# Optimization experiments

Hardware: AMD Instinct MI355X
Metric: run time of the kernel (lower is better)

The kernel has to match this reference:

```python
import jax, jax.numpy as jnp
import numpy as np

T, H, E, K, I = 4096, 1024, 8, 2, 2048
EPS = 1e-5


def setup_inputs() -> dict:
    key = jax.random.key(0)
    ks = jax.random.split(key, 5)
    xavier = jax.nn.initializers.variance_scaling(1.0, 'fan_avg', 'uniform', dtype=jnp.float32)
    return {
        'x': jax.random.normal(ks[0], (T, H), dtype=jnp.float32),
        'scale': jnp.ones((H,), dtype=jnp.float32),
        'gate_kernel': xavier(ks[1], (H, E), jnp.float32),
        'gate_bias': jnp.zeros((E,), dtype=jnp.float32),
        'mlp1_weight': xavier(ks[2], (E, 2 * I, H), jnp.float32),
        'mlp1_bias': jnp.zeros((E, 2 * I), dtype=jnp.float32),
        'mlp2_weight': xavier(ks[3], (E, H, I), jnp.float32),
        'mlp2_bias': jnp.zeros((E, H), dtype=jnp.float32),
    }


def reference(x, scale, gate_kernel, gate_bias, mlp1_weight, mlp1_bias, mlp2_weight, mlp2_bias):
    # RMSNorm in fp32
    t = x.astype(jnp.float32)
    rms = jnp.sqrt(jnp.mean(t * t, axis=-1, keepdims=True) + EPS)
    normed = ((t / rms) * scale).astype(x.dtype)  # [T, H]

    # Gating: top-k experts + softmax over selected logits
    gate_logits = normed @ gate_kernel + gate_bias  # [T, E]
    expert_logits, expert_indices = jax.lax.top_k(gate_logits, K)  # [T, K]
    expert_weights = jax.nn.softmax(expert_logits, axis=-1)  # [T, K]

    # Dense all-expert SwiGLU MLP (faithful to vmap-over-experts original)
    # mlp1_weight: [E, 2I, H] -> mlp1: [E, T, 2I]
    mlp1 = jnp.einsum('td,efd->etf', normed, mlp1_weight) + mlp1_bias[:, None, :]
    gate_part = jnp.minimum(mlp1[..., :I], 7.0)
    linear_part = jnp.clip(mlp1[..., I:], -7.0, 7.0)
    swish_gate = gate_part * jax.nn.sigmoid(1.702 * gate_part)
    activated = swish_gate * (linear_part + 1.0)  # [E, T, I]
    # mlp2_weight: [E, H, I] -> expert_outputs: [T, E, H]
    expert_outputs = (jnp.einsum('eti,ehi->eth', activated, mlp2_weight)
                      + mlp2_bias[:, None, :]).transpose(1, 0, 2)

    # Scatter top-k weights to dense [T, E] and combine
    one_hot = jax.nn.one_hot(expert_indices, E, dtype=expert_outputs.dtype)  # [T, K, E]
    dense_gate_weights = jnp.sum(one_hot * expert_weights[..., None], axis=1)  # [T, E]
    fused = jnp.einsum('teh,te->th', expert_outputs, dense_gate_weights)
    return x + fused
```

## Files before the change

### kernel.cpp

```cpp
#include <hip/hip_runtime.h>
#include <hip/hip_bf16.h>
#include <math.h>

#define T_ 4096
#define H_ 1024
#define E_ 8
#define I_ 2048
#define EPS_ 1e-5f

using bf16x8 = __attribute__((ext_vector_type(8))) short;
using f32x4  = __attribute__((ext_vector_type(4))) float;

static __device__ __forceinline__ unsigned short f2bf(float f) {
    union { float f; unsigned int u; } v; v.f = f;
    unsigned int u = v.u;
    u += 0x7fffu + ((u >> 16) & 1u);
    return (unsigned short)(u >> 16);
}

static __device__ __forceinline__ void gld16(const unsigned short* g, unsigned short* l) {
    __builtin_amdgcn_global_load_lds(
        (const __attribute__((address_space(1))) unsigned int*)g,
        (__attribute__((address_space(3))) unsigned int*)l,
        16, 0, 0);
}

__global__ __launch_bounds__(256) void k_convert(
    const float* __restrict__ src, unsigned short* __restrict__ dst)
{
    size_t i = (size_t)blockIdx.x * 256 + threadIdx.x;
    const float4* s = (const float4*)src + i * 2;
    float4 a = s[0], b = s[1];
    ushort4 lo, hi;
    lo.x = f2bf(a.x); lo.y = f2bf(a.y); lo.z = f2bf(a.z); lo.w = f2bf(a.w);
    hi.x = f2bf(b.x); hi.y = f2bf(b.y); hi.z = f2bf(b.z); hi.w = f2bf(b.w);
    ((ushort4*)dst)[i * 2]     = lo;
    ((ushort4*)dst)[i * 2 + 1] = hi;
}

__global__ __launch_bounds__(256) void k_norm_gate(
    const float* __restrict__ x, const float* __restrict__ scale,
    const float* __restrict__ gk, const float* __restrict__ gb,
    unsigned short* __restrict__ normed_bf,
    int* __restrict__ counts, int* __restrict__ tok_list, float* __restrict__ wtok)
{
    int tid = threadIdx.x;
    int wave = tid >> 6, lane = tid & 63;
    int t = blockIdx.x * 4 + wave;
    const float* xr = x + (size_t)t * H_;
    int h0 = lane * 16;

    float4 xv[4], sv[4];
    #pragma unroll
    for (int c = 0; c < 4; c++) {
        xv[c] = *(const float4*)(xr + h0 + c * 4);
        sv[c] = *(const float4*)(scale + h0 + c * 4);
    }
    float ss = 0.f;
    #pragma unroll
    for (int c = 0; c < 4; c++)
        ss += xv[c].x*xv[c].x + xv[c].y*xv[c].y + xv[c].z*xv[c].z + xv[c].w*xv[c].w;
    #pragma unroll
    for (int off = 32; off; off >>= 1) ss += __shfl_xor(ss, off);
    float inv = 1.0f / sqrtf(ss / (float)H_ + EPS_);

    float nv[16];
    #pragma unroll
    for (int c = 0; c < 4; c++) {
        nv[c*4+0] = xv[c].x * inv * sv[c].x;
        nv[c*4+1] = xv[c].y * inv * sv[c].y;
        nv[c*4+2] = xv[c].z * inv * sv[c].z;
        nv[c*4+3] = xv[c].w * inv * sv[c].w;
    }
    #pragma unroll
    for (int c = 0; c < 4; c++) {
        ushort4 nb;
        nb.x = f2bf(nv[c*4+0]); nb.y = f2bf(nv[c*4+1]);
        nb.z = f2bf(nv[c*4+2]); nb.w = f2bf(nv[c*4+3]);
        *(ushort4*)(normed_bf + (size_t)t * H_ + h0 + c * 4) = nb;
    }

    float p[E_];
    #pragma unroll
    for (int e = 0; e < E_; e++) p[e] = 0.f;
    #pragma unroll
    for (int j = 0; j < 16; j++) {
        const float4* g4 = (const float4*)(gk + (size_t)(h0 + j) * E_);
        float4 a = g4[0], b = g4[1];
        float n = nv[j];
        p[0] += n*a.x; p[1] += n*a.y; p[2] += n*a.z; p[3] += n*a.w;
        p[4] += n*b.x; p[5] += n*b.y; p[6] += n*b.z; p[7] += n*b.w;
    }
    #pragma unroll
    for (int e = 0; e < E_; e++) {
        #pragma unroll
        for (int off = 32; off; off >>= 1) p[e] += __shfl_xor(p[e], off);
    }
    if (lane == 0) {
        int b0 = -1, b1 = -1; float l0 = -1e30f, l1 = -1e30f;
        #pragma unroll
        for (int e = 0; e < E_; e++) {
            float lg = p[e] + gb[e];
            if (lg > l0) { l1 = l0; b1 = b0; l0 = lg; b0 = e; }
            else if (lg > l1) { l1 = lg; b1 = e; }
        }
        float e1 = expf(l1 - l0);
        float w0 = 1.f / (1.f + e1);
        float w1 = e1 / (1.f + e1);
        wtok[t * 2 + 0] = w0;
        wtok[t * 2 + 1] = w1;
        int p0 = atomicAdd(&counts[b0], 1);
        tok_list[b0 * T_ + p0] = t * 2 + 0;
        int p1 = atomicAdd(&counts[b1], 1);
        tok_list[b1 * T_ + p1] = t * 2 + 1;
    }
}

__global__ __launch_bounds__(256) void k_mlp1(
    const unsigned short* __restrict__ w1b,
    const float* __restrict__ b1,
    const unsigned short* __restrict__ normed_bf,
    const int* __restrict__ counts, const int* __restrict__ tok_list,
    unsigned short* __restrict__ act)
{
    int e = blockIdx.z;
    int Ne = counts[e];
    int mt0 = blockIdx.y * 128;
    if (mt0 >= Ne) return;
    int it0 = blockIdx.x * 64;
    int tid = threadIdx.x;
    int lane = tid & 63, w = tid >> 6;
    int quad = lane >> 4, m16 = lane & 15;
    int wr = w >> 1, wc = w & 1;

    __shared__ unsigned short lA[2][128 * 64];
    __shared__ unsigned short lBg[2][64 * 64];
    __shared__ unsigned short lBl[2][64 * 64];
    __shared__ int ls_tk[128];

    if (tid < 128) {
        int slot = mt0 + tid;
        ls_tk[tid] = (slot < Ne) ? tok_list[e * T_ + slot] : -1;
    }

    int lr = lane >> 3;
    int pc = lane & 7;

    const unsigned short* srcA[4];
    #pragma unroll
    for (int it = 0; it < 4; it++) {
        int r = w * 32 + it * 8 + lr;
        int slot = mt0 + r;
        int tk = (slot < Ne) ? tok_list[e * T_ + slot] : 0;
        srcA[it] = normed_bf + (size_t)(tk >> 1) * H_ + ((pc ^ (r & 7)) << 3);
    }
    const size_t w1base = (size_t)e * 2 * I_ * H_;
    const unsigned short* srcG[2];
    const unsigned short* srcL[2];
    #pragma unroll
    for (int it = 0; it < 2; it++) {
        int r = w * 16 + it * 8 + lr;
        srcG[it] = w1b + w1base + (size_t)(it0 + r) * H_ + ((pc ^ (r & 7)) << 3);
        srcL[it] = srcG[it] + (size_t)I_ * H_;
    }

    f32x4 accg[4][2], accl[4][2];
    #pragma unroll
    for (int mi = 0; mi < 4; mi++)
        #pragma unroll
        for (int ni = 0; ni < 2; ni++) {
            accg[mi][ni] = (f32x4){0.f, 0.f, 0.f, 0.f};
            accl[mi][ni] = (f32x4){0.f, 0.f, 0.f, 0.f};
        }

    int m7 = m16 & 7;

#define STAGE1(buf, kk)                                                       \
    {                                                                          \
        _Pragma("unroll")                                                      \
        for (int it = 0; it < 4; it++)                                         \
            gld16(srcA[it] + (kk), &lA[buf][(w * 32 + it * 8) * 64]);          \
        _Pragma("unroll")                                                      \
        for (int it = 0; it < 2; it++) {                                       \
            gld16(srcG[it] + (kk), &lBg[buf][(w * 16 + it * 8) * 64]);         \
            gld16(srcL[it] + (kk), &lBl[buf][(w * 16 + it * 8) * 64]);         \
        }                                                                      \
    }

#define COMP1(buf)                                                             \
    {                                                                          \
        _Pragma("unroll")                                                      \
        for (int ks = 0; ks < 2; ks++) {                                       \
            int jj = ks * 4 + quad;                                            \
            bf16x8 af[4], bg[2], bl[2];                                        \
            _Pragma("unroll")                                                  \
            for (int mi = 0; mi < 4; mi++)                                     \
                af[mi] = *(const bf16x8*)(&lA[buf][(wr * 64 + mi * 16 + m16) * 64 + ((jj ^ m7) << 3)]); \
            _Pragma("unroll")                                                  \
            for (int ni = 0; ni < 2; ni++) {                                   \
                bg[ni] = *(const bf16x8*)(&lBg[buf][(wc * 32 + ni * 16 + m16) * 64 + ((jj ^ m7) << 3)]); \
                bl[ni] = *(const bf16x8*)(&lBl[buf][(wc * 32 + ni * 16 + m16) * 64 + ((jj ^ m7) << 3)]); \
            }                                                                  \
            _Pragma("unroll")                                                  \
            for (int mi = 0; mi < 4; mi++)                                     \
                _Pragma("unroll")                                              \
                for (int ni = 0; ni < 2; ni++) {                               \
                    accg[mi][ni] = __builtin_amdgcn_mfma_f32_16x16x32_bf16(    \
                        af[mi], bg[ni], accg[mi][ni], 0, 0, 0);                \
                    accl[mi][ni] = __builtin_amdgcn_mfma_f32_16x16x32_bf16(    \
                        af[mi], bl[ni], accl[mi][ni], 0, 0, 0);                \
                }                                                              \
        }                                                                      \
    }

    STAGE1(0, 0);
    __syncthreads();
    for (int kk = 0; kk < H_; kk += 128) {
        STAGE1(1, kk + 64);
        COMP1(0);
        __syncthreads();
        if (kk + 128 < H_) STAGE1(0, kk + 128);
        COMP1(1);
        __syncthreads();
    }
#undef STAGE1
#undef COMP1

    const float* b1g = b1 + (size_t)e * 2 * I_;
    const float* b1l = b1g + I_;
    #pragma unroll
    for (int mi = 0; mi < 4; mi++) {
        #pragma unroll
        for (int reg = 0; reg < 4; reg++) {
            int row = wr * 64 + mi * 16 + quad * 4 + reg;
            int tk = ls_tk[row];
            if (tk < 0) continue;
            #pragma unroll
            for (int ni = 0; ni < 2; ni++) {
                int i = it0 + wc * 32 + ni * 16 + m16;
                float g = accg[mi][ni][reg] + b1g[i];
                float l = accl[mi][ni][reg] + b1l[i];
                g = fminf(g, 7.f);
                l = fminf(fmaxf(l, -7.f), 7.f);
                float sw = g / (1.f + expf(-1.702f * g));
                act[(size_t)tk * I_ + i] = f2bf(sw * (l + 1.f));
            }
        }
    }
}

__global__ __launch_bounds__(256) void k_mlp2(
    const unsigned short* __restrict__ w2b,
    const float* __restrict__ b2,
    const unsigned short* __restrict__ act,
    const int* __restrict__ counts, const int* __restrict__ tok_list,
    float* __restrict__ ybuf)
{
    int e = blockIdx.z;
    int Ne = counts[e];
    int mt0 = blockIdx.y * 128;
    if (mt0 >= Ne) return;
    int ht0 = blockIdx.x * 128;
    int tid = threadIdx.x;
    int lane = tid & 63, w = tid >> 6;
    int quad = lane >> 4, m16 = lane & 15;
    int wr = w >> 1, wc = w & 1;

    __shared__ unsigned short lA[2][128 * 64];
    __shared__ unsigned short lB[2][128 * 64];
    __shared__ int ls_tk[128];

    if (tid < 128) {
        int slot = mt0 + tid;
        ls_tk[tid] = (slot < Ne) ? tok_list[e * T_ + slot] : -1;
    }

    int lr = lane >> 3;
    int pc = lane & 7;

    const unsigned short* srcA[4];
    #pragma unroll
    for (int it = 0; it < 4; it++) {
        int r = w * 32 + it * 8 + lr;
        int slot = mt0 + r;
        int tk = (slot < Ne) ? tok_list[e * T_ + slot] : 0;
        srcA[it] = act + (size_t)tk * I_ + ((pc ^ (r & 7)) << 3);
    }
    const size_t w2base = (size_t)e * H_ * I_;
    const unsigned short* srcB[4];
    #pragma unroll
    for (int it = 0; it < 4; it++) {
        int r = w * 32 + it * 8 + lr;
        srcB[it] = w2b + w2base + (size_t)(ht0 + r) * I_ + ((pc ^ (r & 7)) << 3);
    }

    f32x4 acc[4][4];
    #pragma unroll
    for (int mi = 0; mi < 4; mi++)
        #pragma unroll
        for (int ni = 0; ni < 4; ni++)
            acc[mi][ni] = (f32x4){0.f, 0.f, 0.f, 0.f};

    int m7 = m16 & 7;

#define STAGE2(buf, kk)                                                       \
    {                                                                          \
        _Pragma("unroll")                                                      \
        for (int it = 0; it < 4; it++)                                         \
            gld16(srcA[it] + (kk), &lA[buf][(w * 32 + it * 8) * 64]);          \
        _Pragma("unroll")                                                      \
        for (int it = 0; it < 4; it++)                                         \
            gld16(srcB[it] + (kk), &lB[buf][(w * 32 + it * 8) * 64]);          \
    }

#define COMP2(buf)                                                             \
    {                                                                          \
        _Pragma("unroll")                                                      \
        for (int ks = 0; ks < 2; ks++) {                                       \
            int jj = ks * 4 + quad;                                            \
            bf16x8 af[4], bv[4];                                               \
            _Pragma("unroll")                                                  \
            for (int mi = 0; mi < 4; mi++)                                     \
                af[mi] = *(const bf16x8*)(&lA[buf][(wr * 64 + mi * 16 + m16) * 64 + ((jj ^ m7) << 3)]); \
            _Pragma("unroll")                                                  \
            for (int ni = 0; ni < 4; ni++)                                     \
                bv[ni] = *(const bf16x8*)(&lB[buf][(wc * 64 + ni * 16 + m16) * 64 + ((jj ^ m7) << 3)]); \
            _Pragma("unroll")                                                  \
            for (int mi = 0; mi < 4; mi++)                                     \
                _Pragma("unroll")                                              \
                for (int ni = 0; ni < 4; ni++)                                 \
                    acc[mi][ni] = __builtin_amdgcn_mfma_f32_16x16x32_bf16(     \
                        af[mi], bv[ni], acc[mi][ni], 0, 0, 0);                 \
        }                                                                      \
    }

    STAGE2(0, 0);
    __syncthreads();
    for (int kk = 0; kk < I_; kk += 128) {
        STAGE2(1, kk + 64);
        COMP2(0);
        __syncthreads();
        if (kk + 128 < I_) STAGE2(0, kk + 128);
        COMP2(1);
        __syncthreads();
    }
#undef STAGE2
#undef COMP2

    const float* b2e = b2 + (size_t)e * H_;
    #pragma unroll
    for (int mi = 0; mi < 4; mi++) {
        #pragma unroll
        for (int reg = 0; reg < 4; reg++) {
            int row = wr * 64 + mi * 16 + quad * 4 + reg;
            int tk = ls_tk[row];
            if (tk < 0) continue;
            #pragma unroll
            for (int ni = 0; ni < 4; ni++) {
                int h = ht0 + wc * 64 + ni * 16 + m16;
                ybuf[(size_t)tk * H_ + h] = acc[mi][ni][reg] + b2e[h];
            }
        }
    }
}

__global__ __launch_bounds__(256) void k_combine(
    const float* __restrict__ x, const float* __restrict__ ybuf,
    const float* __restrict__ wtok, float* __restrict__ out)
{
    int t = blockIdx.x;
    int tid = threadIdx.x;
    float w0 = wtok[t * 2 + 0];
    float w1 = wtok[t * 2 + 1];
    float4 xv = ((const float4*)(x + (size_t)t * H_))[tid];
    float4 y0 = ((const float4*)(ybuf + (size_t)(t * 2) * H_))[tid];
    float4 y1 = ((const float4*)(ybuf + (size_t)(t * 2 + 1) * H_))[tid];
    float4 o;
    o.x = xv.x + w0 * y0.x + w1 * y1.x;
    o.y = xv.y + w0 * y0.y + w1 * y1.y;
    o.z = xv.z + w0 * y0.z + w1 * y1.z;
    o.w = xv.w + w0 * y0.w + w1 * y1.w;
    ((float4*)(out + (size_t)t * H_))[tid] = o;
}

extern "C" void kernel_launch(void* const* d_in, const int* in_sizes, int n_in,
                              void* d_out, int out_size, void* d_ws, size_t ws_size,
                              hipStream_t stream) {
    const float* x     = (const float*)d_in[0];
    const float* scale = (const float*)d_in[1];
    const float* gk    = (const float*)d_in[2];
    const float* gb    = (const float*)d_in[3];
    const float* w1    = (const float*)d_in[4];
    const float* b1    = (const float*)d_in[5];
    const float* w2    = (const float*)d_in[6];
    const float* b2    = (const float*)d_in[7];
    float* out = (float*)d_out;

    char* ws = (char*)d_ws;
    const size_t MB = 1024 * 1024;
    unsigned short* normed_bf = (unsigned short*)ws;
    unsigned short* act       = (unsigned short*)(ws + 8 * MB);
    unsigned short* w1b       = (unsigned short*)(ws + 40 * MB);
    float*          ybuf      = (float*)(ws + 40 * MB);
    unsigned short* w2b       = (unsigned short*)(ws + 104 * MB);
    char* ctl                 = ws + 136 * MB;
    int*   counts   = (int*)ctl;
    int*   tok_list = (int*)(ctl + 256);
    float* wtok     = (float*)(ctl + 256 + (size_t)E_ * T_ * 4);

    hipMemsetAsync(counts, 0, E_ * sizeof(int), stream);

    k_norm_gate<<<dim3(T_ / 4), dim3(256), 0, stream>>>(
        x, scale, gk, gb, normed_bf, counts, tok_list, wtok);
    k_convert<<<dim3((E_ * 2 * I_ * H_) / (256 * 8)), dim3(256), 0, stream>>>(w1, w1b);
    k_convert<<<dim3((E_ * H_ * I_) / (256 * 8)), dim3(256), 0, stream>>>(w2, w2b);

    k_mlp1<<<dim3(I_ / 64, T_ / 128, E_), dim3(256), 0, stream>>>(
        w1b, b1, normed_bf, counts, tok_list, act);
    k_mlp2<<<dim3(H_ / 128, T_ / 128, E_), dim3(256), 0, stream>>>(
        w2b, b2, act, counts, tok_list, ybuf);
    k_combine<<<dim3(T_), dim3(256), 0, stream>>>(x, ybuf, wtok, out);
}
```

Measured before the change: 609.1 us.

## Enlarge MoE GEMM tiles to 512 threads with ping-pong MFMA scheduling

Both expert GEMM kernels move to 512-thread blocks with 256-row token tiles. mlp1 now computes 128 gate plus 128 linear columns per block in one merged B buffer. The K loop is restructured so each wave splits its MFMA work into sub-blocks separated by raw s_barrier calls, with setprio raised around MFMAs and explicit vmcnt waits, to interleave LDS reads, global prefetch and matrix math across waves. The larger tiles are meant to raise operand reuse and hide latency, at the cost of more LDS per block, more registers, lower occupancy and more wasted rows for experts whose token counts do not fill a tile.

```diff
diff --git a/kernel.cpp b/kernel.cpp
--- a/kernel.cpp
+++ b/kernel.cpp
@@ -24,6 +24,8 @@
         (__attribute__((address_space(3))) unsigned int*)l,
         16, 0, 0);
 }
+
+#define BAR() __builtin_amdgcn_s_barrier()
 
 __global__ __launch_bounds__(256) void k_convert(
     const float* __restrict__ src, unsigned short* __restrict__ dst)
@@ -116,7 +118,7 @@
     }
 }
 
-__global__ __launch_bounds__(256) void k_mlp1(
+__global__ __launch_bounds__(512) void k_mlp1(
     const unsigned short* __restrict__ w1b,
     const float* __restrict__ b1,
     const unsigned short* __restrict__ normed_bf,
@@ -125,20 +127,20 @@
 {
     int e = blockIdx.z;
     int Ne = counts[e];
-    int mt0 = blockIdx.y * 128;
+    int mt0 = blockIdx.y * 256;
     if (mt0 >= Ne) return;
-    int it0 = blockIdx.x * 64;
+    int it0 = blockIdx.x * 128;
     int tid = threadIdx.x;
     int lane = tid & 63, w = tid >> 6;
     int quad = lane >> 4, m16 = lane & 15;
-    int wr = w >> 1, wc = w & 1;
-
-    __shared__ unsigned short lA[2][128 * 64];
-    __shared__ unsigned short lBg[2][64 * 64];
-    __shared__ unsigned short lBl[2][64 * 64];
-    __shared__ int ls_tk[128];
-
-    if (tid < 128) {
+    int wr = w >> 2, wc = w & 3;
+    int m7 = m16 & 7;
+
+    __shared__ unsigned short lA[2][256 * 64];
+    __shared__ unsigned short lB[2][256 * 64];
+    __shared__ int ls_tk[256];
+
+    if (tid < 256) {
         int slot = mt0 + tid;
         ls_tk[tid] = (slot < Ne) ? tok_list[e * T_ + slot] : -1;
     }
@@ -155,101 +157,115 @@
         srcA[it] = normed_bf + (size_t)(tk >> 1) * H_ + ((pc ^ (r & 7)) << 3);
     }
     const size_t w1base = (size_t)e * 2 * I_ * H_;
-    const unsigned short* srcG[2];
-    const unsigned short* srcL[2];
-    #pragma unroll
-    for (int it = 0; it < 2; it++) {
-        int r = w * 16 + it * 8 + lr;
-        srcG[it] = w1b + w1base + (size_t)(it0 + r) * H_ + ((pc ^ (r & 7)) << 3);
-        srcL[it] = srcG[it] + (size_t)I_ * H_;
-    }
-
-    f32x4 accg[4][2], accl[4][2];
-    #pragma unroll
-    for (int mi = 0; mi < 4; mi++)
-        #pragma unroll
-        for (int ni = 0; ni < 2; ni++) {
-            accg[mi][ni] = (f32x4){0.f, 0.f, 0.f, 0.f};
-            accl[mi][ni] = (f32x4){0.f, 0.f, 0.f, 0.f};
-        }
-
-    int m7 = m16 & 7;
-
-#define STAGE1(buf, kk)                                                       \
+    const unsigned short* srcB[4];
+    #pragma unroll
+    for (int it = 0; it < 4; it++) {
+        int r = w * 32 + it * 8 + lr;
+        int col = it0 + ((r >> 6) << 5) + (r & 31);
+        const unsigned short* base = w1b + w1base + ((r & 32) ? (size_t)I_ * H_ : (size_t)0);
+        srcB[it] = base + (size_t)col * H_ + ((pc ^ (r & 7)) << 3);
+    }
+
+    f32x4 acc[8][4];
+    #pragma unroll
+    for (int mi = 0; mi < 8; mi++)
+        #pragma unroll
+        for (int ni = 0; ni < 4; ni++)
+            acc[mi][ni] = (f32x4){0.f, 0.f, 0.f, 0.f};
+
+#define STAGE1(b, koff)                                                        \
     {                                                                          \
         _Pragma("unroll")                                                      \
         for (int it = 0; it < 4; it++)                                         \
-            gld16(srcA[it] + (kk), &lA[buf][(w * 32 + it * 8) * 64]);          \
-        _Pragma("unroll")                                                      \
-        for (int it = 0; it < 2; it++) {                                       \
-            gld16(srcG[it] + (kk), &lBg[buf][(w * 16 + it * 8) * 64]);         \
-            gld16(srcL[it] + (kk), &lBl[buf][(w * 16 + it * 8) * 64]);         \
-        }                                                                      \
-    }
-
-#define COMP1(buf)                                                             \
-    {                                                                          \
-        _Pragma("unroll")                                                      \
-        for (int ks = 0; ks < 2; ks++) {                                       \
-            int jj = ks * 4 + quad;                                            \
-            bf16x8 af[4], bg[2], bl[2];                                        \
+            gld16(srcA[it] + (koff), &lA[b][(w * 32 + it * 8) * 64]);          \
+        _Pragma("unroll")                                                      \
+        for (int it = 0; it < 4; it++)                                         \
+            gld16(srcB[it] + (koff), &lB[b][(w * 32 + it * 8) * 64]);          \
+        __builtin_amdgcn_sched_barrier(0);                                     \
+    }
+
+#define RD_A1(dst, b, pm)                                                      \
+    _Pragma("unroll")                                                          \
+    for (int i = 0; i < 4; i++)                                                \
+        _Pragma("unroll")                                                      \
+        for (int ks = 0; ks < 2; ks++)                                         \
+            dst[i][ks] = *(const bf16x8*)(&lA[b][(wr * 128 + ((pm) * 4 + i) * 16 + m16) * 64 + (((ks * 4 + quad) ^ m7) << 3)]);
+
+#define RD_B1(dst, b, pn)                                                      \
+    _Pragma("unroll")                                                          \
+    for (int i = 0; i < 2; i++)                                                \
+        _Pragma("unroll")                                                      \
+        for (int ks = 0; ks < 2; ks++)                                         \
+            dst[i][ks] = *(const bf16x8*)(&lB[b][(wc * 64 + ((pn) * 2 + i) * 16 + m16) * 64 + (((ks * 4 + quad) ^ m7) << 3)]);
+
+#define MM1(pm, pn, bsrc)                                                      \
+    {                                                                          \
+        __builtin_amdgcn_s_setprio(1);                                         \
+        _Pragma("unroll")                                                      \
+        for (int i = 0; i < 4; i++)                                            \
             _Pragma("unroll")                                                  \
-            for (int mi = 0; mi < 4; mi++)                                     \
-                af[mi] = *(const bf16x8*)(&lA[buf][(wr * 64 + mi * 16 + m16) * 64 + ((jj ^ m7) << 3)]); \
-            _Pragma("unroll")                                                  \
-            for (int ni = 0; ni < 2; ni++) {                                   \
-                bg[ni] = *(const bf16x8*)(&lBg[buf][(wc * 32 + ni * 16 + m16) * 64 + ((jj ^ m7) << 3)]); \
-                bl[ni] = *(const bf16x8*)(&lBl[buf][(wc * 32 + ni * 16 + m16) * 64 + ((jj ^ m7) << 3)]); \
-            }                                                                  \
-            _Pragma("unroll")                                                  \
-            for (int mi = 0; mi < 4; mi++)                                     \
+            for (int j = 0; j < 2; j++)                                        \
                 _Pragma("unroll")                                              \
-                for (int ni = 0; ni < 2; ni++) {                               \
-                    accg[mi][ni] = __builtin_amdgcn_mfma_f32_16x16x32_bf16(    \
-                        af[mi], bg[ni], accg[mi][ni], 0, 0, 0);                \
-                    accl[mi][ni] = __builtin_amdgcn_mfma_f32_16x16x32_bf16(    \
-                        af[mi], bl[ni], accl[mi][ni], 0, 0, 0);                \
-                }                                                              \
-        }                                                                      \
+                for (int ks = 0; ks < 2; ks++)                                 \
+                    acc[(pm) * 4 + i][(pn) * 2 + j] =                          \
+                        __builtin_amdgcn_mfma_f32_16x16x32_bf16(               \
+                            am[i][ks], bsrc[j][ks],                            \
+                            acc[(pm) * 4 + i][(pn) * 2 + j], 0, 0, 0);         \
+        __builtin_amdgcn_s_setprio(0);                                         \
+    }
+
+#define KTILE1(b, do_stage, koff)                                              \
+    {                                                                          \
+        bf16x8 am[4][2], bn0[2][2], bn1[2][2];                                 \
+        RD_A1(am, b, 0); RD_B1(bn0, b, 0);                                     \
+        if (do_stage) STAGE1(1 - (b), koff);                                   \
+        BAR(); MM1(0, 0, bn0); BAR();                                          \
+        RD_B1(bn1, b, 1);                                                      \
+        BAR(); MM1(0, 1, bn1); BAR();                                          \
+        RD_A1(am, b, 1);                                                       \
+        BAR(); MM1(1, 1, bn1); BAR();                                          \
+        MM1(1, 0, bn0);                                                        \
+        asm volatile("s_waitcnt vmcnt(0)" ::: "memory");                       \
+        __builtin_amdgcn_sched_barrier(0);                                     \
+        BAR();                                                                 \
     }
 
     STAGE1(0, 0);
     __syncthreads();
-    for (int kk = 0; kk < H_; kk += 128) {
-        STAGE1(1, kk + 64);
-        COMP1(0);
-        __syncthreads();
-        if (kk + 128 < H_) STAGE1(0, kk + 128);
-        COMP1(1);
-        __syncthreads();
+    for (int t2 = 0; t2 < 16; t2 += 2) {
+        KTILE1(0, true, (t2 + 1) * 64);
+        KTILE1(1, (t2 + 2) < 16, (t2 + 2) * 64);
     }
 #undef STAGE1
-#undef COMP1
+#undef RD_A1
+#undef RD_B1
+#undef MM1
+#undef KTILE1
 
     const float* b1g = b1 + (size_t)e * 2 * I_;
     const float* b1l = b1g + I_;
     #pragma unroll
-    for (int mi = 0; mi < 4; mi++) {
+    for (int mi = 0; mi < 8; mi++) {
         #pragma unroll
         for (int reg = 0; reg < 4; reg++) {
-            int row = wr * 64 + mi * 16 + quad * 4 + reg;
+            int row = wr * 128 + mi * 16 + quad * 4 + reg;
             int tk = ls_tk[row];
             if (tk < 0) continue;
             #pragma unroll
-            for (int ni = 0; ni < 2; ni++) {
-                int i = it0 + wc * 32 + ni * 16 + m16;
-                float g = accg[mi][ni][reg] + b1g[i];
-                float l = accl[mi][ni][reg] + b1l[i];
+            for (int j = 0; j < 2; j++) {
+                int c = it0 + wc * 32 + j * 16 + m16;
+                float g = acc[mi][j][reg]     + b1g[c];
+                float l = acc[mi][2 + j][reg] + b1l[c];
                 g = fminf(g, 7.f);
                 l = fminf(fmaxf(l, -7.f), 7.f);
                 float sw = g / (1.f + expf(-1.702f * g));
-                act[(size_t)tk * I_ + i] = f2bf(sw * (l + 1.f));
+                act[(size_t)tk * I_ + c] = f2bf(sw * (l + 1.f));
             }
         }
     }
 }
 
-__global__ __launch_bounds__(256) void k_mlp2(
+__global__ __launch_bounds__(512) void k_mlp2(
     const unsigned short* __restrict__ w2b,
     const float* __restrict__ b2,
     const unsigned short* __restrict__ act,
@@ -258,19 +274,20 @@
 {
     int e = blockIdx.z;
     int Ne = counts[e];
-    int mt0 = blockIdx.y * 128;
+    int mt0 = blockIdx.y * 256;
     if (mt0 >= Ne) return;
     int ht0 = blockIdx.x * 128;
     int tid = threadIdx.x;
     int lane = tid & 63, w = tid >> 6;
     int quad = lane >> 4, m16 = lane & 15;
     int wr = w >> 1, wc = w & 1;
-
-    __shared__ unsigned short lA[2][128 * 64];
+    int m7 = m16 & 7;
+
+    __shared__ unsigned short lA[2][256 * 64];
     __shared__ unsigned short lB[2][128 * 64];
-    __shared__ int ls_tk[128];
-
-    if (tid < 128) {
+    __shared__ int ls_tk[256];
+
+    if (tid < 256) {
         int slot = mt0 + tid;
         ls_tk[tid] = (slot < Ne) ? tok_list[e * T_ + slot] : -1;
     }
@@ -287,10 +304,10 @@
         srcA[it] = act + (size_t)tk * I_ + ((pc ^ (r & 7)) << 3);
     }
     const size_t w2base = (size_t)e * H_ * I_;
-    const unsigned short* srcB[4];
-    #pragma unroll
-    for (int it = 0; it < 4; it++) {
-        int r = w * 32 + it * 8 + lr;
+    const unsigned short* srcB[2];
+    #pragma unroll
+    for (int it = 0; it < 2; it++) {
+        int r = w * 16 + it * 8 + lr;
         srcB[it] = w2b + w2base + (size_t)(ht0 + r) * I_ + ((pc ^ (r & 7)) << 3);
     }
 
@@ -301,51 +318,70 @@
         for (int ni = 0; ni < 4; ni++)
             acc[mi][ni] = (f32x4){0.f, 0.f, 0.f, 0.f};
 
-    int m7 = m16 & 7;
-
-#define STAGE2(buf, kk)                                                       \
+#define STAGE2(b, koff)                                                        \
     {                                                                          \
         _Pragma("unroll")                                                      \
         for (int it = 0; it < 4; it++)                                         \
-            gld16(srcA[it] + (kk), &lA[buf][(w * 32 + it * 8) * 64]);          \
-        _Pragma("unroll")                                                      \
-        for (int it = 0; it < 4; it++)                                         \
-            gld16(srcB[it] + (kk), &lB[buf][(w * 32 + it * 8) * 64]);          \
-    }
-
-#define COMP2(buf)                                                             \
-    {                                                                          \
-        _Pragma("unroll")                                                      \
-        for (int ks = 0; ks < 2; ks++) {                                       \
-            int jj = ks * 4 + quad;                                            \
-            bf16x8 af[4], bv[4];                                               \
+            gld16(srcA[it] + (koff), &lA[b][(w * 32 + it * 8) * 64]);          \
+        _Pragma("unroll")                                                      \
+        for (int it = 0; it < 2; it++)                                         \
+            gld16(srcB[it] + (koff), &lB[b][(w * 16 + it * 8) * 64]);          \
+        __builtin_amdgcn_sched_barrier(0);                                     \
+    }
+
+#define RD_A2(dst, b)                                                          \
+    _Pragma("unroll")                                                          \
+    for (int i = 0; i < 4; i++)                                                \
+        _Pragma("unroll")                                                      \
+        for (int ks = 0; ks < 2; ks++)                                         \
+            dst[i][ks] = *(const bf16x8*)(&lA[b][(wr * 64 + i * 16 + m16) * 64 + (((ks * 4 + quad) ^ m7) << 3)]);
+
+#define RD_B2(dst, b, pn)                                                      \
+    _Pragma("unroll")                                                          \
+    for (int i = 0; i < 2; i++)                                                \
+        _Pragma("unroll")                                                      \
+        for (int ks = 0; ks < 2; ks++)                                         \
+            dst[i][ks] = *(const bf16x8*)(&lB[b][(wc * 64 + ((pn) * 2 + i) * 16 + m16) * 64 + (((ks * 4 + quad) ^ m7) << 3)]);
+
+#define MM2(pn, bsrc)                                                          \
+    {                                                                          \
+        __builtin_amdgcn_s_setprio(1);                                         \
+        _Pragma("unroll")                                                      \
+        for (int i = 0; i < 4; i++)                                            \
             _Pragma("unroll")                                                  \
-            for (int mi = 0; mi < 4; mi++)                                     \
-                af[mi] = *(const bf16x8*)(&lA[buf][(wr * 64 + mi * 16 + m16) * 64 + ((jj ^ m7) << 3)]); \
-            _Pragma("unroll")                                                  \
-            for (int ni = 0; ni < 4; ni++)                                     \
-                bv[ni] = *(const bf16x8*)(&lB[buf][(wc * 64 + ni * 16 + m16) * 64 + ((jj ^ m7) << 3)]); \
-            _Pragma("unroll")                                                  \
-            for (int mi = 0; mi < 4; mi++)                                     \
+            for (int j = 0; j < 2; j++)                                        \
                 _Pragma("unroll")                                              \
-                for (int ni = 0; ni < 4; ni++)                                 \
-                    acc[mi][ni] = __builtin_amdgcn_mfma_f32_16x16x32_bf16(     \
-                        af[mi], bv[ni], acc[mi][ni], 0, 0, 0);                 \
-        }                                                                      \
+                for (int ks = 0; ks < 2; ks++)                                 \
+                    acc[i][(pn) * 2 + j] =                                     \
+                        __builtin_amdgcn_mfma_f32_16x16x32_bf16(               \
+                            am[i][ks], bsrc[j][ks], acc[i][(pn) * 2 + j], 0, 0, 0); \
+        __builtin_amdgcn_s_setprio(0);                                         \
+    }
+
+#define KTILE2(b, do_stage, koff)                                              \
+    {                                                                          \
+        bf16x8 am[4][2], bn0[2][2], bn1[2][2];                                 \
+        RD_A2(am, b); RD_B2(bn0, b, 0);                                        \
+        if (do_stage) STAGE2(1 - (b), koff);                                   \
+        BAR(); MM2(0, bn0); BAR();                                             \
+        RD_B2(bn1, b, 1);                                                      \
+        BAR(); MM2(1, bn1);                                                    \
+        asm volatile("s_waitcnt vmcnt(0)" ::: "memory");                       \
+        __builtin_amdgcn_sched_barrier(0);                                     \
+        BAR();                                                                 \
     }
 
     STAGE2(0, 0);
     __syncthreads();
-    for (int kk = 0; kk < I_; kk += 128) {
-        STAGE2(1, kk + 64);
-        COMP2(0);
-        __syncthreads();
-        if (kk + 128 < I_) STAGE2(0, kk + 128);
-        COMP2(1);
-        __syncthreads();
+    for (int t2 = 0; t2 < 32; t2 += 2) {
+        KTILE2(0, true, (t2 + 1) * 64);
+        KTILE2(1, (t2 + 2) < 32, (t2 + 2) * 64);
     }
 #undef STAGE2
-#undef COMP2
+#undef RD_A2
+#undef RD_B2
+#undef MM2
+#undef KTILE2
 
     const float* b2e = b2 + (size_t)e * H_;
     #pragma unroll
@@ -415,9 +451,9 @@
     k_convert<<<dim3((E_ * 2 * I_ * H_) / (256 * 8)), dim3(256), 0, stream>>>(w1, w1b);
     k_convert<<<dim3((E_ * H_ * I_) / (256 * 8)), dim3(256), 0, stream>>>(w2, w2b);
 
-    k_mlp1<<<dim3(I_ / 64, T_ / 128, E_), dim3(256), 0, stream>>>(
+    k_mlp1<<<dim3(I_ / 128, T_ / 256, E_), dim3(512), 0, stream>>>(
         w1b, b1, normed_bf, counts, tok_list, act);
-    k_mlp2<<<dim3(H_ / 128, T_ / 128, E_), dim3(256), 0, stream>>>(
+    k_mlp2<<<dim3(H_ / 128, T_ / 256, E_), dim3(512), 0, stream>>>(
         w2b, b2, act, counts, tok_list, ybuf);
     k_combine<<<dim3(T_), dim3(256), 0, stream>>>(x, ybuf, wtok, out);
 }
```

New measurement: 591.2 us. 1.03x faster.
